# Performance work log

Hardware: AMD Instinct MI355X
Metric: run time of the kernel (lower is better)

## Reference

```python
import jax, jax.numpy as jnp
import numpy as np

B, T, C = 8, 2048, 512   # batch, seq_len, channels (= output_size for residual)
H, K, D = 4, 128, 128    # heads, key_size, per-head value size
KS, DIL = 4, 4           # conv kernel size, dilation = kernal_size**block_id
BAND = 3                 # matrix_band_part num_lower = num_upper = 3
NEG = -10000000.0


def setup_inputs() -> dict:
    key = jax.random.key(0)
    ks = jax.random.split(key, 12)
    s = 0.02
    f32 = jnp.float32
    x = jax.random.normal(ks[0], (B, T, C), f32)
    # per-head q/k/v dense params (stacked over head axis)
    Wq = jax.random.normal(ks[1], (H, C, K), f32) * s
    bq = jnp.zeros((H, K), f32)
    Wk = jax.random.normal(ks[2], (H, C, K), f32) * s
    bk = jnp.zeros((H, K), f32)
    Wv = jax.random.normal(ks[3], (H, C, D), f32) * s
    bv = jnp.zeros((H, D), f32)
    # output combiner Dense(output_size)
    Wo = jax.random.normal(ks[4], (H * D, C), f32) * s
    bo = jnp.zeros((C,), f32)
    # causal dilated Conv1D: kernel layout WIO = (kernel, in, out)
    Wc = jax.random.normal(ks[5], (KS, C, C), f32) * s
    bc = jnp.zeros((C,), f32)
    return {"x": x, "Wq": Wq, "bq": bq, "Wk": Wk, "bk": bk,
            "Wv": Wv, "bv": bv, "Wo": Wo, "bo": bo, "Wc": Wc, "bc": bc}


def reference(x, Wq, bq, Wk, bk, Wv, bv, Wo, bo, Wc, bc):
    # per-head projections: [B,H,T,K/D]
    q = jnp.einsum('btc,hck->bhtk', x, Wq) + bq[None, :, None, :]
    k = jnp.einsum('btc,hck->bhtk', x, Wk) + bk[None, :, None, :]
    v = jnp.einsum('btc,hcd->bhtd', x, Wv) + bv[None, :, None, :]
    # dense scores then band mask (faithful to matrix_band_part + abs>0 mask)
    sim = jnp.einsum('bhtk,bhsk->bhts', q, k) / jnp.sqrt(jnp.float32(K))
    idx = jnp.arange(T)
    band = (jnp.abs(idx[:, None] - idx[None, :]) <= BAND).astype(sim.dtype)
    simb = sim * band
    mask = jnp.where(jnp.abs(simb) > 0.0, 0.0, 1.0).astype(sim.dtype)
    att = jax.nn.softmax(simb + NEG * mask, axis=-1)
    heads = jnp.einsum('bhts,bhsd->bhtd', att, v)          # [B,H,T,D]
    cat = heads.transpose(0, 2, 1, 3).reshape(B, T, H * D)  # concat heads
    out = cat @ Wo + bo                                     # Dense(512)
    # causal dilated conv + relu
    pad = (KS - 1) * DIL
    conv = jax.lax.conv_general_dilated(
        out, Wc, window_strides=(1,), padding=[(pad, 0)],
        rhs_dilation=(DIL,), dimension_numbers=('NWC', 'WIO', 'NWC'))
    conv = jax.nn.relu(conv + bc)
    res = conv + x
    return jnp.where(res >= 0, res, 0.2 * res)  # leaky_relu(alpha=0.2)
```

## Files before the change

### kernel.cpp

```cpp
#include <hip/hip_runtime.h>
#include <math.h>

#define Bb    8
#define Tseq  2048
#define Cch   512
#define Mrows 16384
#define Nqkv  1536

typedef __bf16 bf16x8 __attribute__((ext_vector_type(8)));
typedef __bf16 bf16x4 __attribute__((ext_vector_type(4)));
typedef float  f32x4  __attribute__((ext_vector_type(4)));

__device__ __forceinline__ void gld_lds16(const void* g, void* l) {
  __builtin_amdgcn_global_load_lds(
      (const __attribute__((address_space(1))) unsigned int*)g,
      (__attribute__((address_space(3))) unsigned int*)l, 16, 0, 0);
}

#define SWZ(r, g) (((r) << 6) + ((((g) ^ ((r) & 7))) << 3))

__device__ __forceinline__ void swizzle_mn(int* m0, int* n0) {
  const int NX = gridDim.x;
  const int total = NX * gridDim.y;
  const int lid = blockIdx.y * NX + blockIdx.x;
  const int xcd = lid & 7;
  const int chunk = lid >> 3;
  const int idx = xcd * (total >> 3) + chunk;
  const int mt = idx / NX;
  const int nt = idx - mt * NX;
  *m0 = mt * 128;
  *n0 = nt * 128;
}

__global__ __launch_bounds__(256, 2) void gemm_qkv_wp_kernel(
    const __bf16* __restrict__ xb, const __bf16* __restrict__ Wqkv_t,
    const float* __restrict__ bq, const float* __restrict__ bk,
    const float* __restrict__ bv, __bf16* __restrict__ qkv,
    const __bf16* __restrict__ Wc_t, const __bf16* __restrict__ Wob,
    __bf16* __restrict__ Wp_bt) {
  __shared__ __align__(16) __bf16 As[128 * 64];
  __shared__ __align__(16) __bf16 Bs[128 * 64];
  const int tid = threadIdx.x;
  const int w = tid >> 6, lane = tid & 63;
  const int wm = w & 1, wn = w >> 1;
  const int lm = lane & 15, quad = lane >> 4;
  const int srow = lane >> 3;
  const int scol = (((lane & 7) ^ srow) << 3);
  const int lid = blockIdx.x;

  const __bf16 *Ap, *Bp;
  __bf16* op;
  int lda, ldo, m0, n0;
  bool dobias;
  if (lid < 1536) {
    const int xcd = lid & 7, chunk = lid >> 3;
    const int idx = xcd * 192 + chunk;
    const int mt = idx / 12, nt = idx - mt * 12;
    m0 = mt * 128; n0 = nt * 128;
    Ap = xb; lda = 512; Bp = Wqkv_t;
    op = qkv; ldo = 1536; dobias = true;
  } else {
    const int l2 = lid - 1536;
    const int z = l2 >> 4;
    m0 = ((l2 >> 2) & 3) * 128; n0 = (l2 & 3) * 128;
    Ap = Wc_t + z * 512; lda = 2048; Bp = Wob;
    op = Wp_bt + z * 512; ldo = 2048; dobias = false;
  }

  f32x4 acc[4][4] = {};
  for (int k0 = 0; k0 < 512; k0 += 64) {
#pragma unroll
    for (int it = 0; it < 4; ++it) {
      const int c = w * 4 + it;
      const int row = c * 8 + srow;
      gld_lds16(Ap + (size_t)(m0 + row) * lda + k0 + scol, &As[c * 512]);
      gld_lds16(Bp + (size_t)(n0 + row) * 512 + k0 + scol, &Bs[c * 512]);
    }
    __syncthreads();
#pragma unroll
    for (int ks = 0; ks < 2; ++ks) {
      bf16x8 af[4], bfr[4];
#pragma unroll
      for (int i = 0; i < 4; ++i)
        af[i] = *(const bf16x8*)&As[SWZ(wm * 64 + i * 16 + lm, ks * 4 + quad)];
#pragma unroll
      for (int j = 0; j < 4; ++j)
        bfr[j] = *(const bf16x8*)&Bs[SWZ(wn * 64 + j * 16 + lm, ks * 4 + quad)];
#pragma unroll
      for (int i = 0; i < 4; ++i)
#pragma unroll
        for (int j = 0; j < 4; ++j)
          acc[i][j] = __builtin_amdgcn_mfma_f32_16x16x32_bf16(af[i], bfr[j], acc[i][j], 0, 0, 0);
    }
    __syncthreads();
  }
#pragma unroll
  for (int j = 0; j < 4; ++j) {
    const int col = n0 + wn * 64 + j * 16 + lm;
    float bias = 0.f;
    if (dobias) {
      const int s = col >> 9;
      const float* bp = (s == 0) ? bq : (s == 1 ? bk : bv);
      bias = bp[col & 511];
    }
#pragma unroll
    for (int i = 0; i < 4; ++i) {
      const int row0 = m0 + wm * 64 + i * 16 + quad * 4;
#pragma unroll
      for (int r = 0; r < 4; ++r)
        op[(size_t)(row0 + r) * ldo + col] = (__bf16)(acc[i][j][r] + bias);
    }
  }
}

__global__ __launch_bounds__(256, 2) void conv_gemm_kernel(
    const __bf16* __restrict__ A,
    const __bf16* __restrict__ Bt,
    const float* __restrict__ bc, const float* __restrict__ bj,
    const float* __restrict__ x, float* __restrict__ out,
    const __bf16* __restrict__ zeros) {
  __shared__ __align__(16) __bf16 As[128 * 64];
  __shared__ __align__(16) __bf16 Bs[128 * 64];
  const int tid = threadIdx.x;
  const int w = tid >> 6, lane = tid & 63;
  const int wm = w & 1, wn = w >> 1;
  const int lm = lane & 15, quad = lane >> 4;
  const int srow = lane >> 3;
  const int scol = (((lane & 7) ^ srow) << 3);
  int m0, n0;
  swizzle_mn(&m0, &n0);
  f32x4 acc[4][4] = {};
  for (int k0 = 0; k0 < 4 * Cch; k0 += 64) {
    const int jtap = k0 >> 9;
    const int shift = 4 * jtap - 12;
    const int cin0 = k0 & 511;
#pragma unroll
    for (int it = 0; it < 4; ++it) {
      const int c = w * 4 + it;
      const int row = c * 8 + srow;
      const int m = m0 + row;
      const __bf16* src = (((m & (Tseq - 1)) + shift) >= 0)
                              ? A + (size_t)(m + shift) * Cch + cin0 + scol
                              : zeros + scol;
      gld_lds16(src, &As[c * 512]);
      gld_lds16(Bt + (size_t)(n0 + row) * 2048 + k0 + scol, &Bs[c * 512]);
    }
    __syncthreads();
#pragma unroll
    for (int ks = 0; ks < 2; ++ks) {
      bf16x8 af[4], bfr[4];
#pragma unroll
      for (int i = 0; i < 4; ++i)
        af[i] = *(const bf16x8*)&As[SWZ(wm * 64 + i * 16 + lm, ks * 4 + quad)];
#pragma unroll
      for (int j = 0; j < 4; ++j)
        bfr[j] = *(const bf16x8*)&Bs[SWZ(wn * 64 + j * 16 + lm, ks * 4 + quad)];
#pragma unroll
      for (int i = 0; i < 4; ++i)
#pragma unroll
        for (int j = 0; j < 4; ++j)
          acc[i][j] = __builtin_amdgcn_mfma_f32_16x16x32_bf16(af[i], bfr[j], acc[i][j], 0, 0, 0);
    }
    __syncthreads();
  }
#pragma unroll
  for (int j = 0; j < 4; ++j) {
    const int col = n0 + wn * 64 + j * 16 + lm;
    const float bcv = bc[col];
    float suf[4];
    suf[3] = bj[3 * 512 + col];
    suf[2] = suf[3] + bj[2 * 512 + col];
    suf[1] = suf[2] + bj[1 * 512 + col];
    suf[0] = suf[1] + bj[0 * 512 + col];
#pragma unroll
    for (int i = 0; i < 4; ++i) {
      const int row0 = m0 + wm * 64 + i * 16 + quad * 4;
#pragma unroll
      for (int r = 0; r < 4; ++r) {
        const int row = row0 + r;
        const int tl = row & (Tseq - 1);
        int jm = 15 - tl;
        jm = (jm < 0) ? 0 : (jm >> 2);
        float v = acc[i][j][r] + bcv + suf[jm];
        v = fmaxf(v, 0.f);
        v += x[(size_t)row * Cch + col];
        out[(size_t)row * Cch + col] = (v >= 0.f) ? v : 0.2f * v;
      }
    }
  }
}

__global__ __launch_bounds__(256) void attn_band_kernel(
    const __bf16* __restrict__ qkv, __bf16* __restrict__ cat) {
  __shared__ __align__(16) __bf16 ks[70 * 128];
  __shared__ __align__(16) __bf16 vs[70 * 128];
  const int tid = threadIdx.x;
  const int bh = blockIdx.y;
  const int b = bh >> 2, h = bh & 3;
  const int t0 = blockIdx.x * 64;
  for (int c = tid; c < 70 * 16; c += 256) {
    const int row = c >> 4, chunk = c & 15;
    int s = t0 - 3 + row;
    s = (s < 0) ? 0 : ((s > Tseq - 1) ? Tseq - 1 : s);
    const __bf16* src = qkv + ((size_t)(b * Tseq + s)) * Nqkv + 512 + h * 128 + chunk * 8;
    *(bf16x8*)&ks[row * 128 + chunk * 8] = *(const bf16x8*)src;
    *(bf16x8*)&vs[row * 128 + chunk * 8] = *(const bf16x8*)(src + 512);
  }
  __syncthreads();
  const int g = tid & 15, grp = tid >> 4;
  const int d0 = g * 8;
  const float scale = 0.08838834764831845f;
#pragma unroll
  for (int tt = 0; tt < 4; ++tt) {
    const int tl = grp * 4 + tt;
    const int t = t0 + tl;
    bf16x8 qv = *(const bf16x8*)(qkv + ((size_t)(b * Tseq + t)) * Nqkv + h * 128 + d0);
    float score[7];
#pragma unroll
    for (int i = 0; i < 7; ++i) {
      const int s = t - 3 + i;
      const bool valid = (s >= 0) && (s < Tseq);
      bf16x8 kv = *(const bf16x8*)&ks[(tl + i) * 128 + d0];
      float p = 0.f;
#pragma unroll
      for (int e = 0; e < 8; ++e) p += (float)qv[e] * (float)kv[e];
      p += __shfl_xor(p, 1);
      p += __shfl_xor(p, 2);
      p += __shfl_xor(p, 4);
      p += __shfl_xor(p, 8);
      score[i] = valid ? p * scale : -1e30f;
    }
    float mx = score[0];
#pragma unroll
    for (int i = 1; i < 7; ++i) mx = fmaxf(mx, score[i]);
    float wgt[7], denom = 0.f;
#pragma unroll
    for (int i = 0; i < 7; ++i) {
      wgt[i] = (score[i] > -1e29f) ? expf(score[i] - mx) : 0.f;
      denom += wgt[i];
    }
    const float inv = 1.f / denom;
    float o[8] = {};
#pragma unroll
    for (int i = 0; i < 7; ++i) {
      bf16x8 vv = *(const bf16x8*)&vs[(tl + i) * 128 + d0];
#pragma unroll
      for (int e = 0; e < 8; ++e) o[e] += wgt[i] * (float)vv[e];
    }
    bf16x8 ov;
#pragma unroll
    for (int e = 0; e < 8; ++e) ov[e] = (__bf16)(o[e] * inv);
    *(bf16x8*)(cat + ((size_t)(b * Tseq + t)) * Cch + h * 128 + d0) = ov;
  }
}

#define PREP_A 8192
#define PREP_B 8960
#define PREP_C 9984
#define PREP_D 10240
#define PREP_E 10241
#define PREP_N 10273

__global__ __launch_bounds__(256) void prep_kernel(
    const float* __restrict__ x, const float* __restrict__ Wq,
    const float* __restrict__ Wk, const float* __restrict__ Wv,
    const float* __restrict__ Wo, const float* __restrict__ Wc,
    const float* __restrict__ bo,
    __bf16* __restrict__ xb, __bf16* __restrict__ Wqkv_t,
    __bf16* __restrict__ Wc_t, __bf16* __restrict__ Wob,
    float* __restrict__ bj, __bf16* __restrict__ zeros) {
  __shared__ float sArr[32][33];
  __shared__ float red[256];
  const int bid = blockIdx.x;
  const int tid = threadIdx.x;
  if (bid < PREP_A) {
    const size_t i = ((size_t)bid * 256 + tid) * 4;
    float4 v = *(const float4*)(x + i);
    bf16x4 o;
    o[0] = (__bf16)v.x; o[1] = (__bf16)v.y; o[2] = (__bf16)v.z; o[3] = (__bf16)v.w;
    *(bf16x4*)(xb + i) = o;
  } else if (bid < PREP_B) {
    const int l = bid - PREP_A;
    const int bx = l & 3, by = (l >> 2) & 15, z = l >> 6;
    const int sgrp = z >> 2, h = z & 3;
    const float* src = ((sgrp == 0) ? Wq : (sgrp == 1) ? Wk : Wv) + h * (512 * 128);
    __bf16* dst = Wqkv_t + (size_t)z * 128 * 512;
    const int tx = tid & 31, ty = tid >> 5;
    const int c0 = bx * 32, r0 = by * 32;
#pragma unroll
    for (int rr = 0; rr < 4; ++rr)
      sArr[ty + rr * 8][tx] = src[(size_t)(r0 + ty + rr * 8) * 128 + c0 + tx];
    __syncthreads();
#pragma unroll
    for (int rr = 0; rr < 4; ++rr)
      dst[(size_t)(c0 + ty + rr * 8) * 512 + r0 + tx] = (__bf16)sArr[tx][ty + rr * 8];
  } else if (bid < PREP_C) {
    const int l = bid - PREP_B;
    const int bx = l & 15, by = l >> 4;
    const int tx = tid & 31, ty = tid >> 5;
    const int c0 = bx * 32, r0 = by * 32;
#pragma unroll
    for (int rr = 0; rr < 4; ++rr)
      sArr[ty + rr * 8][tx] = Wc[(size_t)(r0 + ty + rr * 8) * 512 + c0 + tx];
    __syncthreads();
#pragma unroll
    for (int rr = 0; rr < 4; ++rr)
      Wc_t[(size_t)(c0 + ty + rr * 8) * 2048 + r0 + tx] = (__bf16)sArr[tx][ty + rr * 8];
  } else if (bid < PREP_D) {
    const int l = bid - PREP_C;
    const size_t i = ((size_t)l * 256 + tid) * 4;
    float4 v = *(const float4*)(Wo + i);
    bf16x4 o;
    o[0] = (__bf16)v.x; o[1] = (__bf16)v.y; o[2] = (__bf16)v.z; o[3] = (__bf16)v.w;
    *(bf16x4*)(Wob + i) = o;
  } else if (bid < PREP_E) {
    bf16x8 zero = {};
    *(bf16x8*)(zeros + tid * 8) = zero;
  } else {
    const int l = bid - PREP_E;
    const int j = l >> 3, nb = l & 7;
    const int n = nb * 64 + (tid & 63);
    const int cig = tid >> 6;
    const float* base = Wc + ((size_t)j * 512 + cig * 128) * 512 + n;
    float acc = 0.f;
#pragma unroll 8
    for (int ci = 0; ci < 128; ++ci) acc += bo[cig * 128 + ci] * base[(size_t)ci * 512];
    red[tid] = acc;
    __syncthreads();
    if (tid < 64)
      bj[j * 512 + n] = red[tid] + red[tid + 64] + red[tid + 128] + red[tid + 192];
  }
}

extern "C" void kernel_launch(void* const* d_in, const int* in_sizes, int n_in,
                              void* d_out, int out_size, void* d_ws, size_t ws_size,
                              hipStream_t stream) {
  const float* x  = (const float*)d_in[0];
  const float* Wq = (const float*)d_in[1];
  const float* bq = (const float*)d_in[2];
  const float* Wk = (const float*)d_in[3];
  const float* bk = (const float*)d_in[4];
  const float* Wv = (const float*)d_in[5];
  const float* bv = (const float*)d_in[6];
  const float* Wo = (const float*)d_in[7];
  const float* bo = (const float*)d_in[8];
  const float* Wc = (const float*)d_in[9];
  const float* bc = (const float*)d_in[10];
  float* out = (float*)d_out;

  char* p = (char*)d_ws;
  __bf16* xb     = (__bf16*)p;  p += (size_t)Mrows * Cch * 2;
  __bf16* qkv    = (__bf16*)p;  p += (size_t)Mrows * Nqkv * 2;
  __bf16* catb   = (__bf16*)p;  p += (size_t)Mrows * Cch * 2;
  __bf16* Wqkv_t = (__bf16*)p;  p += (size_t)Nqkv * Cch * 2;
  __bf16* Wc_t   = (__bf16*)p;  p += (size_t)Cch * 2048 * 2;
  __bf16* Wob    = (__bf16*)p;  p += (size_t)Cch * Cch * 2;
  __bf16* Wp_bt  = (__bf16*)p;  p += (size_t)Cch * 2048 * 2;
  float*  bj     = (float*)p;   p += 4 * Cch * 4;
  __bf16* zeros  = (__bf16*)p;  p += 4096;

  prep_kernel<<<PREP_N, 256, 0, stream>>>(x, Wq, Wk, Wv, Wo, Wc, bo,
                                          xb, Wqkv_t, Wc_t, Wob, bj, zeros);

  gemm_qkv_wp_kernel<<<1600, 256, 0, stream>>>(xb, Wqkv_t, bq, bk, bv, qkv,
                                               Wc_t, Wob, Wp_bt);

  attn_band_kernel<<<dim3(Tseq / 64, Bb * 4), 256, 0, stream>>>(qkv, catb);

  conv_gemm_kernel<<<dim3(Cch / 128, Mrows / 128), 256, 0, stream>>>(
      catb, Wp_bt, bc, bj, x, out, zeros);
}
```

Baseline: 208.0 us.

## Double-buffer LDS tiles in QKV and conv GEMMs to overlap loads with MFMA

Both GEMM kernels now keep two LDS buffers per operand and prefetch the next K-tile with global_load_lds while the current tile is consumed by MFMAs. Explicit vmcnt waits and raw s_barrier replace the __syncthreads pairs, and s_setprio raises wave priority during the MFMA section. This aims to hide global-to-LDS latency that was previously exposed every K step. LDS use doubles to 64KB per block, which may limit occupancy at launch_bounds(256,2), and the hand-written vmcnt counts depend on the exact number of outstanding loads.

```diff
diff --git a/kernel.cpp b/kernel.cpp
--- a/kernel.cpp
+++ b/kernel.cpp
@@ -38,8 +38,8 @@
     const float* __restrict__ bv, __bf16* __restrict__ qkv,
     const __bf16* __restrict__ Wc_t, const __bf16* __restrict__ Wob,
     __bf16* __restrict__ Wp_bt) {
-  __shared__ __align__(16) __bf16 As[128 * 64];
-  __shared__ __align__(16) __bf16 Bs[128 * 64];
+  __shared__ __align__(16) __bf16 As[2][128 * 64];
+  __shared__ __align__(16) __bf16 Bs[2][128 * 64];
   const int tid = threadIdx.x;
   const int w = tid >> 6, lane = tid & 63;
   const int wm = w & 1, wn = w >> 1;
@@ -67,32 +67,49 @@
     op = Wp_bt + z * 512; ldo = 2048; dobias = false;
   }
 
-  f32x4 acc[4][4] = {};
-  for (int k0 = 0; k0 < 512; k0 += 64) {
+  auto stage = [&](int buf, int k0) {
 #pragma unroll
     for (int it = 0; it < 4; ++it) {
       const int c = w * 4 + it;
       const int row = c * 8 + srow;
-      gld_lds16(Ap + (size_t)(m0 + row) * lda + k0 + scol, &As[c * 512]);
-      gld_lds16(Bp + (size_t)(n0 + row) * 512 + k0 + scol, &Bs[c * 512]);
-    }
-    __syncthreads();
+      gld_lds16(Ap + (size_t)(m0 + row) * lda + k0 + scol, &As[buf][c * 512]);
+      gld_lds16(Bp + (size_t)(n0 + row) * 512 + k0 + scol, &Bs[buf][c * 512]);
+    }
+  };
+
+  f32x4 acc[4][4] = {};
+  stage(0, 0);
+  int cur = 0;
+  for (int k0 = 0; k0 < 512; k0 += 64) {
+    if (k0 + 64 < 512) {
+      stage(cur ^ 1, k0 + 64);
+      asm volatile("s_waitcnt vmcnt(8)" ::: "memory");
+    } else {
+      asm volatile("s_waitcnt vmcnt(0)" ::: "memory");
+    }
+    __builtin_amdgcn_s_barrier();
+    asm volatile("" ::: "memory");
+    __builtin_amdgcn_s_setprio(1);
 #pragma unroll
     for (int ks = 0; ks < 2; ++ks) {
       bf16x8 af[4], bfr[4];
 #pragma unroll
       for (int i = 0; i < 4; ++i)
-        af[i] = *(const bf16x8*)&As[SWZ(wm * 64 + i * 16 + lm, ks * 4 + quad)];
+        af[i] = *(const bf16x8*)&As[cur][SWZ(wm * 64 + i * 16 + lm, ks * 4 + quad)];
 #pragma unroll
       for (int j = 0; j < 4; ++j)
-        bfr[j] = *(const bf16x8*)&Bs[SWZ(wn * 64 + j * 16 + lm, ks * 4 + quad)];
+        bfr[j] = *(const bf16x8*)&Bs[cur][SWZ(wn * 64 + j * 16 + lm, ks * 4 + quad)];
 #pragma unroll
       for (int i = 0; i < 4; ++i)
 #pragma unroll
         for (int j = 0; j < 4; ++j)
           acc[i][j] = __builtin_amdgcn_mfma_f32_16x16x32_bf16(af[i], bfr[j], acc[i][j], 0, 0, 0);
     }
-    __syncthreads();
+    __builtin_amdgcn_s_setprio(0);
+    asm volatile("" ::: "memory");
+    __builtin_amdgcn_s_barrier();
+    asm volatile("" ::: "memory");
+    cur ^= 1;
   }
 #pragma unroll
   for (int j = 0; j < 4; ++j) {
@@ -119,8 +136,8 @@
     const float* __restrict__ bc, const float* __restrict__ bj,
     const float* __restrict__ x, float* __restrict__ out,
     const __bf16* __restrict__ zeros) {
-  __shared__ __align__(16) __bf16 As[128 * 64];
-  __shared__ __align__(16) __bf16 Bs[128 * 64];
+  __shared__ __align__(16) __bf16 As[2][128 * 64];
+  __shared__ __align__(16) __bf16 Bs[2][128 * 64];
   const int tid = threadIdx.x;
   const int w = tid >> 6, lane = tid & 63;
   const int wm = w & 1, wn = w >> 1;
@@ -129,8 +146,8 @@
   const int scol = (((lane & 7) ^ srow) << 3);
   int m0, n0;
   swizzle_mn(&m0, &n0);
-  f32x4 acc[4][4] = {};
-  for (int k0 = 0; k0 < 4 * Cch; k0 += 64) {
+
+  auto stage = [&](int buf, int k0) {
     const int jtap = k0 >> 9;
     const int shift = 4 * jtap - 12;
     const int cin0 = k0 & 511;
@@ -142,26 +159,44 @@
       const __bf16* src = (((m & (Tseq - 1)) + shift) >= 0)
                               ? A + (size_t)(m + shift) * Cch + cin0 + scol
                               : zeros + scol;
-      gld_lds16(src, &As[c * 512]);
-      gld_lds16(Bt + (size_t)(n0 + row) * 2048 + k0 + scol, &Bs[c * 512]);
-    }
-    __syncthreads();
+      gld_lds16(src, &As[buf][c * 512]);
+      gld_lds16(Bt + (size_t)(n0 + row) * 2048 + k0 + scol, &Bs[buf][c * 512]);
+    }
+  };
+
+  f32x4 acc[4][4] = {};
+  stage(0, 0);
+  int cur = 0;
+  for (int k0 = 0; k0 < 4 * Cch; k0 += 64) {
+    if (k0 + 64 < 4 * Cch) {
+      stage(cur ^ 1, k0 + 64);
+      asm volatile("s_waitcnt vmcnt(8)" ::: "memory");
+    } else {
+      asm volatile("s_waitcnt vmcnt(0)" ::: "memory");
+    }
+    __builtin_amdgcn_s_barrier();
+    asm volatile("" ::: "memory");
+    __builtin_amdgcn_s_setprio(1);
 #pragma unroll
     for (int ks = 0; ks < 2; ++ks) {
       bf16x8 af[4], bfr[4];
 #pragma unroll
       for (int i = 0; i < 4; ++i)
-        af[i] = *(const bf16x8*)&As[SWZ(wm * 64 + i * 16 + lm, ks * 4 + quad)];
+        af[i] = *(const bf16x8*)&As[cur][SWZ(wm * 64 + i * 16 + lm, ks * 4 + quad)];
 #pragma unroll
       for (int j = 0; j < 4; ++j)
-        bfr[j] = *(const bf16x8*)&Bs[SWZ(wn * 64 + j * 16 + lm, ks * 4 + quad)];
+        bfr[j] = *(const bf16x8*)&Bs[cur][SWZ(wn * 64 + j * 16 + lm, ks * 4 + quad)];
 #pragma unroll
       for (int i = 0; i < 4; ++i)
 #pragma unroll
         for (int j = 0; j < 4; ++j)
           acc[i][j] = __builtin_amdgcn_mfma_f32_16x16x32_bf16(af[i], bfr[j], acc[i][j], 0, 0, 0);
     }
-    __syncthreads();
+    __builtin_amdgcn_s_setprio(0);
+    asm volatile("" ::: "memory");
+    __builtin_amdgcn_s_barrier();
+    asm volatile("" ::: "memory");
+    cur ^= 1;
   }
 #pragma unroll
   for (int j = 0; j < 4; ++j) {
```

After: 211.5 us. No clear change (+1.7%).
